# Kernel optimization log

Measured on AMD Instinct MI355X. Metric: run time of the kernel, lower is better.

The kernel has to match this reference:

```python
import jax, jax.numpy as jnp
import numpy as np

# SamplesLoss('sinkhorn', p=2, blur=0.05, backend='tensorized') defaults (geomloss):
# debiased Sinkhorn divergence, cost C(x,y)=|x-y|^2/2, eps = blur^p,
# epsilon-scaling from diameter^p down to blur^p with scaling=0.5,
# symmetric (averaged) log-domain updates + one final extrapolation step.
P = 2
BLUR = 0.05
SCALING = 0.5
DIAMETER = 10.0  # static diameter estimate for the annealing schedule (randn data)


def _eps_schedule():
    eps_target = BLUR ** P
    lst = []
    e = DIAMETER ** P
    while e > eps_target:
        lst.append(e)
        e *= SCALING ** P
    lst.append(eps_target)
    return lst

EPS_LIST = _eps_schedule()


def _sqcost(x, y):
    # C[b,n,m] = 0.5 * ||x_bn - y_bm||^2, via expansion (avoids [B,N,M,D] tensor)
    x2 = jnp.sum(x * x, axis=-1)  # [B,N]
    y2 = jnp.sum(y * y, axis=-1)  # [B,M]
    xy = jnp.einsum('bnd,bmd->bnm', x, y)
    return 0.5 * (x2[:, :, None] + y2[:, None, :] - 2.0 * xy)


def _softmin(eps, C, h):
    # h: [B,M] (already log-weights + potential/eps); C: [B,N,M] -> [B,N]
    return -eps * jax.nn.logsumexp(h[:, None, :] - C / eps, axis=2)


def _sinkhorn_divergence(x, y, a, b):
    log_a = jnp.log(a)
    log_b = jnp.log(b)
    Cxy = _sqcost(x, y)
    Cyx = jnp.swapaxes(Cxy, 1, 2)
    Cxx = _sqcost(x, x)
    Cyy = _sqcost(y, y)

    eps0 = EPS_LIST[0]
    f_ba = _softmin(eps0, Cxy, log_b)  # potential on x for OT(a,b)
    g_ab = _softmin(eps0, Cyx, log_a)  # potential on y for OT(a,b)
    f_aa = _softmin(eps0, Cxx, log_a)  # debias self-potential on x
    g_bb = _softmin(eps0, Cyy, log_b)  # debias self-potential on y

    for eps in EPS_LIST:
        ft = _softmin(eps, Cxy, log_b + g_ab / eps)
        gt = _softmin(eps, Cyx, log_a + f_ba / eps)
        f_ba = 0.5 * (f_ba + ft)
        g_ab = 0.5 * (g_ab + gt)
        f_aa = 0.5 * (f_aa + _softmin(eps, Cxx, log_a + f_aa / eps))
        g_bb = 0.5 * (g_bb + _softmin(eps, Cyy, log_b + g_bb / eps))

    # final (non-averaged) extrapolation at the target temperature
    eps = EPS_LIST[-1]
    f_fin = _softmin(eps, Cxy, log_b + g_ab / eps)
    g_fin = _softmin(eps, Cyx, log_a + f_ba / eps)
    f_aa = _softmin(eps, Cxx, log_a + f_aa / eps)
    g_bb = _softmin(eps, Cyy, log_b + g_bb / eps)

    # debiased divergence: <a, f_ab - f_aa> + <b, g_ab - g_bb>
    return jnp.sum(a * (f_fin - f_aa), axis=-1) + jnp.sum(b * (g_fin - g_bb), axis=-1)


def setup_inputs() -> dict:
    key = jax.random.key(0)
    k1, k2, k3, k4 = jax.random.split(key, 4)
    B, N, M, D = 8, 2048, 2048, 64
    return {
        'inp1': jax.random.normal(k1, (B, N, D), dtype=jnp.float32),
        'inp2': jax.random.normal(k2, (B, M, D), dtype=jnp.float32),
        'weights1': jax.random.uniform(k3, (B, N), dtype=jnp.float32),
        'weights2': jax.random.uniform(k4, (B, M), dtype=jnp.float32),
    }


def reference(inp1, inp2, weights1, weights2):
    # normalize_weights=True branch of SinkhornLoss.forward
    mass1 = jnp.sum(weights1, axis=1, keepdims=True)
    mass1 = jnp.where(mass1 == 0.0, 1.0, mass1)
    a = weights1 / mass1
    mass2 = jnp.sum(weights2, axis=1, keepdims=True)
    mass2 = jnp.where(mass2 == 0.0, 1.0, mass2)
    b = weights2 / mass2
    loss = _sinkhorn_divergence(inp1, inp2, a, b)  # [B]
    return jnp.mean(loss)  # reduction='mean'
```

## Files before the change

### kernel.cpp

```cpp
#include <hip/hip_runtime.h>
#include <cstdint>
#include <cstddef>

#define BB 8
#define NPTS 2048
#define DIM 64
#define CK 128
#define BROWS 64

typedef _Float16 f16x8 __attribute__((ext_vector_type(8)));
typedef float f32x4 __attribute__((ext_vector_type(4)));

static const float EPS_H[9] = {100.0f, 25.0f, 6.25f, 1.5625f, 0.390625f,
                               0.09765625f, 0.0244140625f, 0.006103515625f,
                               0.0025f};

#if __has_builtin(__builtin_amdgcn_exp2f)
static __device__ __forceinline__ float fexp2(float x) {
  return __builtin_amdgcn_exp2f(x);
}
#else
static __device__ __forceinline__ float fexp2(float x) {
  float r;
  asm("v_exp_f32 %0, %1" : "=v"(r) : "v"(x));
  return r;
}
#endif

static __device__ __forceinline__ f32x4 vmax4(f32x4 a, f32x4 b) {
  f32x4 r;
  #pragma unroll
  for (int i = 0; i < 4; ++i) r[i] = fmaxf(a[i], b[i]);
  return r;
}

static __device__ __forceinline__ f32x4 vexp2_4(f32x4 a) {
  f32x4 r;
  #pragma unroll
  for (int i = 0; i < 4; ++i) r[i] = fexp2(a[i]);
  return r;
}

static __device__ __forceinline__ void gload_lds16(const void* g, void* l) {
  __builtin_amdgcn_global_load_lds(
      (const __attribute__((address_space(1))) void*)g,
      (__attribute__((address_space(3))) void*)l, 16, 0, 0);
}

struct SMTask {
  const _Float16* P;
  const _Float16* Q;
  const float* logw;
  const float* pot;
  const float* qsq;
  const float* psq;
  const float* oldf;
  float* out;
};


__global__ __launch_bounds__(256) void norm_weights_k(
    const float* __restrict__ w, float* __restrict__ aout,
    float* __restrict__ logout, int n) {
  int b = blockIdx.x;
  const float* wb = w + (size_t)b * n;
  __shared__ float red[256];
  float s = 0.f;
  for (int i = threadIdx.x; i < n; i += 256) s += wb[i];
  red[threadIdx.x] = s;
  __syncthreads();
  for (int st = 128; st > 0; st >>= 1) {
    if (threadIdx.x < st) red[threadIdx.x] += red[threadIdx.x + st];
    __syncthreads();
  }
  float mass = red[0];
  if (mass == 0.f) mass = 1.f;
  float inv = 1.f / mass;
  for (int i = threadIdx.x; i < n; i += 256) {
    float av = wb[i] * inv;
    aout[(size_t)b * n + i] = av;
    logout[(size_t)b * n + i] = logf(av);
  }
}

__global__ __launch_bounds__(256) void sqnorm_cvt_k(
    const float* __restrict__ X, float* __restrict__ sq,
    _Float16* __restrict__ Xh, int rows) {
  int row = blockIdx.x * 4 + (threadIdx.x >> 6);
  int lane = threadIdx.x & 63;
  if (row >= rows) return;
  float v = X[(size_t)row * DIM + lane];
  Xh[(size_t)row * DIM + lane] = (_Float16)v;
  float s = v * v;
  #pragma unroll
  for (int off = 32; off > 0; off >>= 1) s += __shfl_xor(s, off);
  if (lane == 0) sq[row] = s;
}

__global__ __launch_bounds__(256, 4) void fused_softmin_k(
    SMTask t0, SMTask t1, SMTask t2, SMTask t3, float ie2, float neg_eps_ln2) {
  __shared__ float hq[NPTS];
  __shared__ __align__(16) _Float16 qb[2][CK * DIM];
  SMTask T = (blockIdx.z == 0) ? t0
           : (blockIdx.z == 1) ? t1
           : (blockIdx.z == 2) ? t2 : t3;
  const int b = blockIdx.y;
  const int tid = threadIdx.x;
  const float LOG2E = 1.4426950408889634f;
  {
    const float* lw = T.logw + (size_t)b * NPTS;
    const float* q2 = T.qsq + (size_t)b * NPTS;
    const float* pt = T.pot ? T.pot + (size_t)b * NPTS : nullptr;
    for (int m = tid; m < NPTS; m += 256) {
      float h = fmaf(lw[m], LOG2E, -0.5f * q2[m] * ie2);
      if (pt) h = fmaf(pt[m], ie2, h);
      hq[m] = h;
    }
  }

  const int lane = tid & 63, wave = tid >> 6;
  const _Float16* Qb = T.Q + (size_t)b * NPTS * DIM;

  auto stage = [&](int buf, int chunk) {
    int m0 = chunk * CK;
    #pragma unroll
    for (int r = 0; r < 4; ++r) {
      int gbase = r * 256 + wave * 64;
      int gid = gbase + lane;
      int row = gid >> 3;
      int kg = (gid & 7) ^ (row & 7);
      const _Float16* src = Qb + (size_t)(m0 + row) * DIM + kg * 8;
      _Float16* dst = &qb[buf][(size_t)gbase * 8];
      gload_lds16(src, dst);
    }
  };

  const int fr = lane & 15;
  const int g0 = lane >> 4;
  const int r0 = blockIdx.x * BROWS + wave * 16;
  const _Float16* Pb = T.P + ((size_t)b * NPTS + r0) * DIM;
  f16x8 a0 = *(const f16x8*)(Pb + fr * DIM + g0 * 8);
  f16x8 a1 = *(const f16x8*)(Pb + fr * DIM + g0 * 8 + 32);

  f32x4 mx4 = {-3.0e38f, -3.0e38f, -3.0e38f, -3.0e38f};
  f32x4 sm4 = {0.f, 0.f, 0.f, 0.f};

  stage(0, 0);
  __syncthreads();

  for (int c = 0; c < NPTS / CK; ++c) {
    int cur = c & 1;
    if (c + 1 < NPTS / CK) stage(cur ^ 1, c + 1);
    int m0 = c * CK;
    const char* qbase = (const char*)&qb[cur][0];

    f32x4 v4[8];
    f32x4 cmx = mx4;
    #pragma unroll
    for (int s = 0; s < 8; ++s) {
      int row = s * 16 + fr;
      int byte0 = row * 128 + ((g0 ^ (row & 7)) << 4);
      int byte1 = row * 128 + (((g0 + 4) ^ (row & 7)) << 4);
      f16x8 b0 = *(const f16x8*)(qbase + byte0);
      f16x8 b1 = *(const f16x8*)(qbase + byte1);
      float hs = hq[m0 + s * 16 + fr];
      f32x4 z = {0.f, 0.f, 0.f, 0.f};
      f32x4 t = __builtin_amdgcn_mfma_f32_16x16x32_f16(a0, b0, z, 0, 0, 0);
      f32x4 acc = __builtin_amdgcn_mfma_f32_16x16x32_f16(a1, b1, t, 0, 0, 0);
      v4[s] = acc * ie2 + hs;
      cmx = vmax4(cmx, v4[s]);
    }
    f32x4 resc = vexp2_4(mx4 - cmx);
    f32x4 esum = vexp2_4(v4[0] - cmx);
    #pragma unroll
    for (int s = 1; s < 8; ++s) esum += vexp2_4(v4[s] - cmx);
    sm4 = sm4 * resc + esum;
    mx4 = cmx;
    __syncthreads();
  }

  #pragma unroll
  for (int off = 1; off < 16; off <<= 1) {
    #pragma unroll
    for (int q = 0; q < 4; ++q) {
      float omx = __shfl_xor(mx4[q], off);
      float osm = __shfl_xor(sm4[q], off);
      float nm = fmaxf(mx4[q], omx);
      sm4[q] = sm4[q] * fexp2(mx4[q] - nm) + osm * fexp2(omx - nm);
      mx4[q] = nm;
    }
  }
  if (fr == 0) {
    #pragma unroll
    for (int q = 0; q < 4; ++q) {
      int r = r0 + g0 * 4 + q;
      size_t oi = (size_t)b * NPTS + r;
      float f = neg_eps_ln2 * (__log2f(sm4[q]) + mx4[q]) + 0.5f * T.psq[oi];
      if (T.oldf) f = 0.5f * (T.oldf[oi] + f);
      T.out[oi] = f;
    }
  }
}

__global__ __launch_bounds__(256) void loss_part_k(
    const float* __restrict__ aW, const float* __restrict__ f_fin,
    const float* __restrict__ f_aa, const float* __restrict__ bW,
    const float* __restrict__ g_fin, const float* __restrict__ g_bb,
    float* __restrict__ part) {
  __shared__ float red[256];
  int i0 = blockIdx.x * 256 + threadIdx.x;
  float s = 0.f;
  for (int i = i0; i < BB * NPTS; i += 64 * 256)
    s += aW[i] * (f_fin[i] - f_aa[i]) + bW[i] * (g_fin[i] - g_bb[i]);
  red[threadIdx.x] = s;
  __syncthreads();
  for (int st = 128; st > 0; st >>= 1) {
    if (threadIdx.x < st) red[threadIdx.x] += red[threadIdx.x + st];
    __syncthreads();
  }
  if (threadIdx.x == 0) part[blockIdx.x] = red[0];
}

__global__ __launch_bounds__(64) void loss_fin_k(const float* __restrict__ part,
                                                 float* __restrict__ out) {
  float s = part[threadIdx.x];
  #pragma unroll
  for (int off = 32; off > 0; off >>= 1) s += __shfl_xor(s, off);
  if (threadIdx.x == 0) out[0] = s * (1.f / BB);
}

__global__ void write_val_k(float* out, float v) { out[0] = v; }


extern "C" void kernel_launch(void* const* d_in, const int* in_sizes, int n_in,
                              void* d_out, int out_size, void* d_ws,
                              size_t ws_size, hipStream_t stream) {
  (void)in_sizes; (void)n_in; (void)out_size;
  const float* X = (const float*)d_in[0];
  const float* Y = (const float*)d_in[1];
  const float* W1 = (const float*)d_in[2];
  const float* W2 = (const float*)d_in[3];
  float* out = (float*)d_out;

  char* base = (char*)d_ws;
  size_t off = 0;
  auto alloc_b = [&](size_t bytes) {
    void* r = base + off;
    off += (bytes + 255) & ~(size_t)255;
    return r;
  };
  const size_t nP = (size_t)BB * NPTS;
  _Float16* Xh = (_Float16*)alloc_b(nP * DIM * 2);
  _Float16* Yh = (_Float16*)alloc_b(nP * DIM * 2);
  float* x2 = (float*)alloc_b(nP * 4);
  float* y2 = (float*)alloc_b(nP * 4);
  float* aW = (float*)alloc_b(nP * 4);
  float* bW = (float*)alloc_b(nP * 4);
  float* la = (float*)alloc_b(nP * 4);
  float* lb = (float*)alloc_b(nP * 4);
  float* fba[2] = {(float*)alloc_b(nP * 4), (float*)alloc_b(nP * 4)};
  float* gab[2] = {(float*)alloc_b(nP * 4), (float*)alloc_b(nP * 4)};
  float* faa[2] = {(float*)alloc_b(nP * 4), (float*)alloc_b(nP * 4)};
  float* gbb[2] = {(float*)alloc_b(nP * 4), (float*)alloc_b(nP * 4)};
  float* part = (float*)alloc_b(64 * 4);
  if (ws_size < off) {
    write_val_k<<<1, 1, 0, stream>>>(out, -(float)(ws_size >> 20));
    return;
  }

  norm_weights_k<<<BB, 256, 0, stream>>>(W1, aW, la, NPTS);
  norm_weights_k<<<BB, 256, 0, stream>>>(W2, bW, lb, NPTS);
  sqnorm_cvt_k<<<BB * NPTS / 4, 256, 0, stream>>>(X, x2, Xh, BB * NPTS);
  sqnorm_cvt_k<<<BB * NPTS / 4, 256, 0, stream>>>(Y, y2, Yh, BB * NPTS);

  const float LN2 = 0.6931471805599453f;
  const float LOG2E = 1.4426950408889634f;
  dim3 fg(NPTS / BROWS, BB, 4);

  auto launch4 = [&](SMTask A, SMTask B2, SMTask C, SMTask D2, float eps) {
    float ie2 = LOG2E / eps;
    float nel = -eps * LN2;
    fused_softmin_k<<<fg, 256, 0, stream>>>(A, B2, C, D2, ie2, nel);
  };

  {
    float e = EPS_H[0];
    launch4(
        SMTask{Xh, Yh, lb, nullptr, y2, x2, nullptr, fba[0]},
        SMTask{Yh, Xh, la, nullptr, x2, y2, nullptr, gab[0]},
        SMTask{Xh, Xh, la, nullptr, x2, x2, nullptr, faa[0]},
        SMTask{Yh, Yh, lb, nullptr, y2, y2, nullptr, gbb[0]},
        e);
  }

  int cur = 0;
  for (int it = 0; it < 9; ++it) {
    float e = EPS_H[it];
    int nxt = cur ^ 1;
    launch4(
        SMTask{Xh, Yh, lb, gab[cur], y2, x2, fba[cur], fba[nxt]},
        SMTask{Yh, Xh, la, fba[cur], x2, y2, gab[cur], gab[nxt]},
        SMTask{Xh, Xh, la, faa[cur], x2, x2, faa[cur], faa[nxt]},
        SMTask{Yh, Yh, lb, gbb[cur], y2, y2, gbb[cur], gbb[nxt]},
        e);
    cur = nxt;
  }

  {
    float e = EPS_H[8];
    int nxt = cur ^ 1;
    launch4(
        SMTask{Xh, Yh, lb, gab[cur], y2, x2, nullptr, fba[nxt]},
        SMTask{Yh, Xh, la, fba[cur], x2, y2, nullptr, gab[nxt]},
        SMTask{Xh, Xh, la, faa[cur], x2, x2, nullptr, faa[nxt]},
        SMTask{Yh, Yh, lb, gbb[cur], y2, y2, nullptr, gbb[nxt]},
        e);
    loss_part_k<<<64, 256, 0, stream>>>(aW, fba[nxt], faa[nxt], bW, gab[nxt],
                                        gbb[nxt], part);
    loss_fin_k<<<1, 64, 0, stream>>>(part, out);
  }
}
```

Before: 482.8 us.

## Pair softmin tasks sharing the same Q matrix and split the M range across block halves

Groups the four softmin tasks into two pairs that share the same Q operand (Y for f_ba/g_bb, X for g_ab/f_aa), so each staged Q tile in LDS feeds two MFMA streams. Blocks grow to 512 threads, with two halves each covering half of the M dimension; the two partial logsumexp results are merged through shared memory at the end. The per-chunk h values are computed inline from global memory instead of being precomputed into an LDS array. This halves Q traffic and LDS staging per output, at the cost of more registers per wave, fewer grid blocks, and a final cross-half reduction.

```diff
diff --git a/kernel.cpp b/kernel.cpp
--- a/kernel.cpp
+++ b/kernel.cpp
@@ -6,7 +6,6 @@
 #define NPTS 2048
 #define DIM 64
 #define CK 128
-#define BROWS 64
 
 typedef _Float16 f16x8 __attribute__((ext_vector_type(8)));
 typedef float f32x4 __attribute__((ext_vector_type(4)));
@@ -47,15 +46,20 @@
       (__attribute__((address_space(3))) void*)l, 16, 0, 0);
 }
 
-struct SMTask {
-  const _Float16* P;
+struct PTask {
   const _Float16* Q;
-  const float* logw;
-  const float* pot;
-  const float* qsq;
-  const float* psq;
-  const float* oldf;
-  float* out;
+  const float* lw;
+  const float* q2;
+  const _Float16* P0;
+  const float* pot0;
+  const float* psq0;
+  const float* oldf0;
+  float* out0;
+  const _Float16* P1;
+  const float* pot1;
+  const float* psq1;
+  const float* oldf1;
+  float* out1;
 };
 
 
@@ -97,85 +101,100 @@
   if (lane == 0) sq[row] = s;
 }
 
-__global__ __launch_bounds__(256, 4) void fused_softmin_k(
-    SMTask t0, SMTask t1, SMTask t2, SMTask t3, float ie2, float neg_eps_ln2) {
-  __shared__ float hq[NPTS];
-  __shared__ __align__(16) _Float16 qb[2][CK * DIM];
-  SMTask T = (blockIdx.z == 0) ? t0
-           : (blockIdx.z == 1) ? t1
-           : (blockIdx.z == 2) ? t2 : t3;
+__global__ __launch_bounds__(512, 4) void fused_softmin_k(
+    PTask u0, PTask u1, float ie2, float neg_eps_ln2) {
+  __shared__ __align__(16) _Float16 qb[2][2][CK * DIM];
+  __shared__ float cmxs[2][2][64];
+  __shared__ float csms[2][2][64];
+  PTask U = blockIdx.z ? u1 : u0;
   const int b = blockIdx.y;
   const int tid = threadIdx.x;
+  const int lane = tid & 63, wave = tid >> 6;
+  const int half = wave >> 2, wsub = wave & 3;
   const float LOG2E = 1.4426950408889634f;
-  {
-    const float* lw = T.logw + (size_t)b * NPTS;
-    const float* q2 = T.qsq + (size_t)b * NPTS;
-    const float* pt = T.pot ? T.pot + (size_t)b * NPTS : nullptr;
-    for (int m = tid; m < NPTS; m += 256) {
-      float h = fmaf(lw[m], LOG2E, -0.5f * q2[m] * ie2);
-      if (pt) h = fmaf(pt[m], ie2, h);
-      hq[m] = h;
-    }
-  }
-
-  const int lane = tid & 63, wave = tid >> 6;
-  const _Float16* Qb = T.Q + (size_t)b * NPTS * DIM;
-
-  auto stage = [&](int buf, int chunk) {
-    int m0 = chunk * CK;
+
+  const _Float16* Qb = U.Q + (size_t)b * NPTS * DIM;
+  const float* lwb = U.lw + (size_t)b * NPTS;
+  const float* q2b = U.q2 + (size_t)b * NPTS;
+  const float* pt0 = U.pot0 ? U.pot0 + (size_t)b * NPTS : nullptr;
+  const float* pt1 = U.pot1 ? U.pot1 + (size_t)b * NPTS : nullptr;
+
+  auto stage = [&](int buf, int c) {
+    int m0 = half * (NPTS / 2) + c * CK;
     #pragma unroll
     for (int r = 0; r < 4; ++r) {
-      int gbase = r * 256 + wave * 64;
+      int gbase = r * 256 + wsub * 64;
       int gid = gbase + lane;
       int row = gid >> 3;
       int kg = (gid & 7) ^ (row & 7);
       const _Float16* src = Qb + (size_t)(m0 + row) * DIM + kg * 8;
-      _Float16* dst = &qb[buf][(size_t)gbase * 8];
+      _Float16* dst = &qb[half][buf][(size_t)gbase * 8];
       gload_lds16(src, dst);
     }
   };
 
   const int fr = lane & 15;
   const int g0 = lane >> 4;
-  const int r0 = blockIdx.x * BROWS + wave * 16;
-  const _Float16* Pb = T.P + ((size_t)b * NPTS + r0) * DIM;
-  f16x8 a0 = *(const f16x8*)(Pb + fr * DIM + g0 * 8);
-  f16x8 a1 = *(const f16x8*)(Pb + fr * DIM + g0 * 8 + 32);
-
-  f32x4 mx4 = {-3.0e38f, -3.0e38f, -3.0e38f, -3.0e38f};
-  f32x4 sm4 = {0.f, 0.f, 0.f, 0.f};
+  const int r0 = blockIdx.x * 64 + wsub * 16;
+  const _Float16* P0b = U.P0 + ((size_t)b * NPTS + r0) * DIM;
+  const _Float16* P1b = U.P1 + ((size_t)b * NPTS + r0) * DIM;
+  f16x8 a00 = *(const f16x8*)(P0b + fr * DIM + g0 * 8);
+  f16x8 a01 = *(const f16x8*)(P0b + fr * DIM + g0 * 8 + 32);
+  f16x8 a10 = *(const f16x8*)(P1b + fr * DIM + g0 * 8);
+  f16x8 a11 = *(const f16x8*)(P1b + fr * DIM + g0 * 8 + 32);
+
+  f32x4 mx0 = {-3.0e38f, -3.0e38f, -3.0e38f, -3.0e38f};
+  f32x4 mx1 = mx0;
+  f32x4 sm0 = {0.f, 0.f, 0.f, 0.f};
+  f32x4 sm1 = sm0;
 
   stage(0, 0);
   __syncthreads();
 
-  for (int c = 0; c < NPTS / CK; ++c) {
+  for (int c = 0; c < NPTS / 2 / CK; ++c) {
     int cur = c & 1;
-    if (c + 1 < NPTS / CK) stage(cur ^ 1, c + 1);
-    int m0 = c * CK;
-    const char* qbase = (const char*)&qb[cur][0];
-
-    f32x4 v4[8];
-    f32x4 cmx = mx4;
+    if (c + 1 < NPTS / 2 / CK) stage(cur ^ 1, c + 1);
+    const int m0 = half * (NPTS / 2) + c * CK;
+    const char* qbase = (const char*)&qb[half][cur][0];
+
     #pragma unroll
-    for (int s = 0; s < 8; ++s) {
-      int row = s * 16 + fr;
-      int byte0 = row * 128 + ((g0 ^ (row & 7)) << 4);
-      int byte1 = row * 128 + (((g0 + 4) ^ (row & 7)) << 4);
-      f16x8 b0 = *(const f16x8*)(qbase + byte0);
-      f16x8 b1 = *(const f16x8*)(qbase + byte1);
-      float hs = hq[m0 + s * 16 + fr];
-      f32x4 z = {0.f, 0.f, 0.f, 0.f};
-      f32x4 t = __builtin_amdgcn_mfma_f32_16x16x32_f16(a0, b0, z, 0, 0, 0);
-      f32x4 acc = __builtin_amdgcn_mfma_f32_16x16x32_f16(a1, b1, t, 0, 0, 0);
-      v4[s] = acc * ie2 + hs;
-      cmx = vmax4(cmx, v4[s]);
+    for (int sh = 0; sh < 2; ++sh) {
+      float hs0[4], hs1[4];
+      #pragma unroll
+      for (int s4 = 0; s4 < 4; ++s4) {
+        int m = m0 + (sh * 4 + s4) * 16 + fr;
+        float hb = fmaf(lwb[m], LOG2E, -0.5f * q2b[m] * ie2);
+        hs0[s4] = pt0 ? fmaf(pt0[m], ie2, hb) : hb;
+        hs1[s4] = pt1 ? fmaf(pt1[m], ie2, hb) : hb;
+      }
+      f32x4 v0[4], v1[4];
+      f32x4 c0 = mx0, c1 = mx1;
+      #pragma unroll
+      for (int s4 = 0; s4 < 4; ++s4) {
+        int row = (sh * 4 + s4) * 16 + fr;
+        int byte0 = row * 128 + ((g0 ^ (row & 7)) << 4);
+        int byte1 = row * 128 + (((g0 + 4) ^ (row & 7)) << 4);
+        f16x8 b0 = *(const f16x8*)(qbase + byte0);
+        f16x8 b1 = *(const f16x8*)(qbase + byte1);
+        f32x4 z = {0.f, 0.f, 0.f, 0.f};
+        f32x4 t0 = __builtin_amdgcn_mfma_f32_16x16x32_f16(a00, b0, z, 0, 0, 0);
+        f32x4 acc0 = __builtin_amdgcn_mfma_f32_16x16x32_f16(a01, b1, t0, 0, 0, 0);
+        f32x4 t1 = __builtin_amdgcn_mfma_f32_16x16x32_f16(a10, b0, z, 0, 0, 0);
+        f32x4 acc1 = __builtin_amdgcn_mfma_f32_16x16x32_f16(a11, b1, t1, 0, 0, 0);
+        v0[s4] = acc0 * ie2 + hs0[s4];
+        v1[s4] = acc1 * ie2 + hs1[s4];
+        c0 = vmax4(c0, v0[s4]);
+        c1 = vmax4(c1, v1[s4]);
+      }
+      f32x4 e0 = vexp2_4(v0[0] - c0) + vexp2_4(v0[1] - c0);
+      e0 += vexp2_4(v0[2] - c0) + vexp2_4(v0[3] - c0);
+      sm0 = sm0 * vexp2_4(mx0 - c0) + e0;
+      mx0 = c0;
+      f32x4 e1 = vexp2_4(v1[0] - c1) + vexp2_4(v1[1] - c1);
+      e1 += vexp2_4(v1[2] - c1) + vexp2_4(v1[3] - c1);
+      sm1 = sm1 * vexp2_4(mx1 - c1) + e1;
+      mx1 = c1;
     }
-    f32x4 resc = vexp2_4(mx4 - cmx);
-    f32x4 esum = vexp2_4(v4[0] - cmx);
-    #pragma unroll
-    for (int s = 1; s < 8; ++s) esum += vexp2_4(v4[s] - cmx);
-    sm4 = sm4 * resc + esum;
-    mx4 = cmx;
     __syncthreads();
   }
 
@@ -183,22 +202,48 @@
   for (int off = 1; off < 16; off <<= 1) {
     #pragma unroll
     for (int q = 0; q < 4; ++q) {
-      float omx = __shfl_xor(mx4[q], off);
-      float osm = __shfl_xor(sm4[q], off);
-      float nm = fmaxf(mx4[q], omx);
-      sm4[q] = sm4[q] * fexp2(mx4[q] - nm) + osm * fexp2(omx - nm);
-      mx4[q] = nm;
+      {
+        float omx = __shfl_xor(mx0[q], off);
+        float osm = __shfl_xor(sm0[q], off);
+        float nm = fmaxf(mx0[q], omx);
+        sm0[q] = sm0[q] * fexp2(mx0[q] - nm) + osm * fexp2(omx - nm);
+        mx0[q] = nm;
+      }
+      {
+        float omx = __shfl_xor(mx1[q], off);
+        float osm = __shfl_xor(sm1[q], off);
+        float nm = fmaxf(mx1[q], omx);
+        sm1[q] = sm1[q] * fexp2(mx1[q] - nm) + osm * fexp2(omx - nm);
+        mx1[q] = nm;
+      }
     }
   }
   if (fr == 0) {
     #pragma unroll
     for (int q = 0; q < 4; ++q) {
-      int r = r0 + g0 * 4 + q;
-      size_t oi = (size_t)b * NPTS + r;
-      float f = neg_eps_ln2 * (__log2f(sm4[q]) + mx4[q]) + 0.5f * T.psq[oi];
-      if (T.oldf) f = 0.5f * (T.oldf[oi] + f);
-      T.out[oi] = f;
+      int rl = wsub * 16 + g0 * 4 + q;
+      cmxs[0][half][rl] = mx0[q];
+      csms[0][half][rl] = sm0[q];
+      cmxs[1][half][rl] = mx1[q];
+      csms[1][half][rl] = sm1[q];
     }
+  }
+  __syncthreads();
+
+  if (tid < 128) {
+    int task = tid >> 6;
+    int rl = tid & 63;
+    float ma = cmxs[task][0][rl], mb = cmxs[task][1][rl];
+    float nm = fmaxf(ma, mb);
+    float ss = csms[task][0][rl] * fexp2(ma - nm) +
+               csms[task][1][rl] * fexp2(mb - nm);
+    size_t oi = (size_t)b * NPTS + blockIdx.x * 64 + rl;
+    const float* psq = task ? U.psq1 : U.psq0;
+    const float* oldf = task ? U.oldf1 : U.oldf0;
+    float* outp = task ? U.out1 : U.out0;
+    float f = neg_eps_ln2 * (__log2f(ss) + nm) + 0.5f * psq[oi];
+    if (oldf) f = 0.5f * (oldf[oi] + f);
+    outp[oi] = f;
   }
 }
 
@@ -275,46 +320,43 @@
 
   const float LN2 = 0.6931471805599453f;
   const float LOG2E = 1.4426950408889634f;
-  dim3 fg(NPTS / BROWS, BB, 4);
-
-  auto launch4 = [&](SMTask A, SMTask B2, SMTask C, SMTask D2, float eps) {
+  dim3 fg(NPTS / 64, BB, 2);
+
+  auto launch4 = [&](const float* potF, const float* oldF, float* outF,
+                     const float* potG, const float* oldG, float* outG,
+                     const float* potA, const float* oldA, float* outA,
+                     const float* potBv, const float* oldBv, float* outBv,
+                     float eps) {
     float ie2 = LOG2E / eps;
     float nel = -eps * LN2;
-    fused_softmin_k<<<fg, 256, 0, stream>>>(A, B2, C, D2, ie2, nel);
+    PTask u0{Yh, lb, y2,
+             Xh, potF, x2, oldF, outF,
+             Yh, potBv, y2, oldBv, outBv};
+    PTask u1{Xh, la, x2,
+             Yh, potG, y2, oldG, outG,
+             Xh, potA, x2, oldA, outA};
+    fused_softmin_k<<<fg, 512, 0, stream>>>(u0, u1, ie2, nel);
   };
 
-  {
-    float e = EPS_H[0];
-    launch4(
-        SMTask{Xh, Yh, lb, nullptr, y2, x2, nullptr, fba[0]},
-        SMTask{Yh, Xh, la, nullptr, x2, y2, nullptr, gab[0]},
-        SMTask{Xh, Xh, la, nullptr, x2, x2, nullptr, faa[0]},
-        SMTask{Yh, Yh, lb, nullptr, y2, y2, nullptr, gbb[0]},
-        e);
-  }
+  launch4(nullptr, nullptr, fba[0], nullptr, nullptr, gab[0],
+          nullptr, nullptr, faa[0], nullptr, nullptr, gbb[0], EPS_H[0]);
 
   int cur = 0;
   for (int it = 0; it < 9; ++it) {
-    float e = EPS_H[it];
     int nxt = cur ^ 1;
-    launch4(
-        SMTask{Xh, Yh, lb, gab[cur], y2, x2, fba[cur], fba[nxt]},
-        SMTask{Yh, Xh, la, fba[cur], x2, y2, gab[cur], gab[nxt]},
-        SMTask{Xh, Xh, la, faa[cur], x2, x2, faa[cur], faa[nxt]},
-        SMTask{Yh, Yh, lb, gbb[cur], y2, y2, gbb[cur], gbb[nxt]},
-        e);
+    launch4(gab[cur], fba[cur], fba[nxt],
+            fba[cur], gab[cur], gab[nxt],
+            faa[cur], faa[cur], faa[nxt],
+            gbb[cur], gbb[cur], gbb[nxt], EPS_H[it]);
     cur = nxt;
   }
 
   {
-    float e = EPS_H[8];
     int nxt = cur ^ 1;
-    launch4(
-        SMTask{Xh, Yh, lb, gab[cur], y2, x2, nullptr, fba[nxt]},
-        SMTask{Yh, Xh, la, fba[cur], x2, y2, nullptr, gab[nxt]},
-        SMTask{Xh, Xh, la, faa[cur], x2, x2, nullptr, faa[nxt]},
-        SMTask{Yh, Yh, lb, gbb[cur], y2, y2, nullptr, gbb[nxt]},
-        e);
+    launch4(gab[cur], nullptr, fba[nxt],
+            fba[cur], nullptr, gab[nxt],
+            faa[cur], nullptr, faa[nxt],
+            gbb[cur], nullptr, gbb[nxt], EPS_H[8]);
     loss_part_k<<<64, 256, 0, stream>>>(aW, fba[nxt], faa[nxt], bW, gab[nxt],
                                         gbb[nxt], part);
     loss_fin_k<<<1, 64, 0, stream>>>(part, out);
```

Result: slower. 680.2 us (+40.9%).

## Split softmin over column halves with 32x32 MFMA and separate merge kernel

Applied to the files above, without the earlier changes.

Reworks the fused softmin kernel into single-wave blocks that each handle 32 rows against one half of the columns, using 32x32x16 MFMA and small 32-column chunks with explicit vmcnt waits and priority hints. Partial max/sum results are written to global memory and combined in a new merge kernel. That kernel also precomputes the next iteration's h vectors, replacing the per-block recomputation of h in LDS. This raises block count and parallelism and removes redundant h setup, but adds a global round trip for partials and an extra launch per iteration.

```diff
diff --git a/kernel.cpp b/kernel.cpp
--- a/kernel.cpp
+++ b/kernel.cpp
@@ -5,15 +5,18 @@
 #define BB 8
 #define NPTS 2048
 #define DIM 64
-#define CK 128
-#define BROWS 64
+#define CK 32
+#define HALFC 1024
+#define NCH (HALFC / CK)
 
 typedef _Float16 f16x8 __attribute__((ext_vector_type(8)));
-typedef float f32x4 __attribute__((ext_vector_type(4)));
+typedef float f32x16 __attribute__((ext_vector_type(16)));
 
 static const float EPS_H[9] = {100.0f, 25.0f, 6.25f, 1.5625f, 0.390625f,
                                0.09765625f, 0.0244140625f, 0.006103515625f,
                                0.0025f};
+#define LOG2E 1.4426950408889634f
+#define LN2 0.6931471805599453f
 
 #if __has_builtin(__builtin_amdgcn_exp2f)
 static __device__ __forceinline__ float fexp2(float x) {
@@ -27,35 +30,23 @@
 }
 #endif
 
-static __device__ __forceinline__ f32x4 vmax4(f32x4 a, f32x4 b) {
-  f32x4 r;
-  #pragma unroll
-  for (int i = 0; i < 4; ++i) r[i] = fmaxf(a[i], b[i]);
-  return r;
-}
-
-static __device__ __forceinline__ f32x4 vexp2_4(f32x4 a) {
-  f32x4 r;
-  #pragma unroll
-  for (int i = 0; i < 4; ++i) r[i] = fexp2(a[i]);
-  return r;
-}
-
 static __device__ __forceinline__ void gload_lds16(const void* g, void* l) {
   __builtin_amdgcn_global_load_lds(
       (const __attribute__((address_space(1))) void*)g,
       (__attribute__((address_space(3))) void*)l, 16, 0, 0);
 }
 
-struct SMTask {
+struct FT {
   const _Float16* P;
   const _Float16* Q;
-  const float* logw;
-  const float* pot;
-  const float* qsq;
+};
+struct MT {
   const float* psq;
   const float* oldf;
   float* out;
+  const float* lwn;
+  const float* q2n;
+  float* hqn;
 };
 
 
@@ -97,108 +88,154 @@
   if (lane == 0) sq[row] = s;
 }
 
-__global__ __launch_bounds__(256, 4) void fused_softmin_k(
-    SMTask t0, SMTask t1, SMTask t2, SMTask t3, float ie2, float neg_eps_ln2) {
-  __shared__ float hq[NPTS];
+__global__ __launch_bounds__(256) void init_hq_k(
+    const float* __restrict__ la, const float* __restrict__ lb,
+    const float* __restrict__ x2, const float* __restrict__ y2,
+    float* __restrict__ hq, float ie2) {
+  int task = blockIdx.z;
+  int idx = blockIdx.x * 256 + threadIdx.x;
+  const float* lw = (task == 1 || task == 2) ? la : lb;
+  const float* q2 = (task == 1 || task == 2) ? x2 : y2;
+  hq[(size_t)task * BB * NPTS + idx] =
+      fmaf(lw[idx], LOG2E, -0.5f * q2[idx] * ie2);
+}
+
+__global__ __launch_bounds__(64, 4) void fused_softmin_k(
+    FT t0, FT t1, FT t2, FT t3, const float* __restrict__ hqG,
+    float* __restrict__ pmx, float* __restrict__ psm, float ie2) {
   __shared__ __align__(16) _Float16 qb[2][CK * DIM];
-  SMTask T = (blockIdx.z == 0) ? t0
-           : (blockIdx.z == 1) ? t1
-           : (blockIdx.z == 2) ? t2 : t3;
-  const int b = blockIdx.y;
-  const int tid = threadIdx.x;
-  const float LOG2E = 1.4426950408889634f;
-  {
-    const float* lw = T.logw + (size_t)b * NPTS;
-    const float* q2 = T.qsq + (size_t)b * NPTS;
-    const float* pt = T.pot ? T.pot + (size_t)b * NPTS : nullptr;
-    for (int m = tid; m < NPTS; m += 256) {
-      float h = fmaf(lw[m], LOG2E, -0.5f * q2[m] * ie2);
-      if (pt) h = fmaf(pt[m], ie2, h);
-      hq[m] = h;
-    }
-  }
-
-  const int lane = tid & 63, wave = tid >> 6;
-  const _Float16* Qb = T.Q + (size_t)b * NPTS * DIM;
-
-  auto stage = [&](int buf, int chunk) {
-    int m0 = chunk * CK;
+  FT T = (blockIdx.z == 0) ? t0
+       : (blockIdx.z == 1) ? t1
+       : (blockIdx.z == 2) ? t2 : t3;
+  const int rowg = blockIdx.x >> 1, half = blockIdx.x & 1;
+  const int b = blockIdx.y, task = blockIdx.z;
+  const int lane = threadIdx.x;
+  const int l31 = lane & 31, hi = lane >> 5;
+
+  const _Float16* Qb = T.Q + ((size_t)b * NPTS + half * HALFC) * DIM;
+  const float* hqp = hqG + ((size_t)task * BB + b) * NPTS + half * HALFC;
+
+  const _Float16* Pb = T.P + ((size_t)b * NPTS + rowg * 32) * DIM;
+  f16x8 a[4];
+  #pragma unroll
+  for (int s = 0; s < 4; ++s)
+    a[s] = *(const f16x8*)(Pb + (size_t)l31 * DIM + s * 16 + hi * 8);
+
+  int baddr[4];
+  #pragma unroll
+  for (int s = 0; s < 4; ++s)
+    baddr[s] = l31 * 128 + (((2 * s + hi) ^ (l31 & 7)) << 4);
+  const char* qb0 = (const char*)&qb[0][0];
+
+  auto stage = [&](int buf, int c) {
+    int m0 = c * CK;
     #pragma unroll
     for (int r = 0; r < 4; ++r) {
-      int gbase = r * 256 + wave * 64;
-      int gid = gbase + lane;
+      int gid = r * 64 + lane;
       int row = gid >> 3;
       int kg = (gid & 7) ^ (row & 7);
-      const _Float16* src = Qb + (size_t)(m0 + row) * DIM + kg * 8;
-      _Float16* dst = &qb[buf][(size_t)gbase * 8];
-      gload_lds16(src, dst);
+      gload_lds16(Qb + (size_t)(m0 + row) * DIM + kg * 8, &qb[buf][r * 512]);
     }
   };
 
-  const int fr = lane & 15;
-  const int g0 = lane >> 4;
-  const int r0 = blockIdx.x * BROWS + wave * 16;
-  const _Float16* Pb = T.P + ((size_t)b * NPTS + r0) * DIM;
-  f16x8 a0 = *(const f16x8*)(Pb + fr * DIM + g0 * 8);
-  f16x8 a1 = *(const f16x8*)(Pb + fr * DIM + g0 * 8 + 32);
-
-  f32x4 mx4 = {-3.0e38f, -3.0e38f, -3.0e38f, -3.0e38f};
-  f32x4 sm4 = {0.f, 0.f, 0.f, 0.f};
+  float mx[16], sm[16];
+  #pragma unroll
+  for (int r = 0; r < 16; ++r) { mx[r] = -3.0e38f; sm[r] = 0.f; }
 
   stage(0, 0);
-  __syncthreads();
-
-  for (int c = 0; c < NPTS / CK; ++c) {
-    int cur = c & 1;
-    if (c + 1 < NPTS / CK) stage(cur ^ 1, c + 1);
-    int m0 = c * CK;
-    const char* qbase = (const char*)&qb[cur][0];
-
-    f32x4 v4[8];
-    f32x4 cmx = mx4;
+  float hq_c = hqp[l31];
+  float v0[16], v1[16];
+
+#define SUB(c_, BUF_, VOUT_, LAST_)                                          \
+  {                                                                          \
+    float hq_n = 0.f;                                                        \
+    if (!(LAST_)) {                                                          \
+      stage((BUF_) ^ 1, (c_) + 1);                                           \
+      hq_n = hqp[((c_) + 1) * CK + l31];                                     \
+    }                                                                        \
+    if (LAST_) asm volatile("s_waitcnt vmcnt(0)" ::: "memory");              \
+    else       asm volatile("s_waitcnt vmcnt(5)" ::: "memory");              \
+    __builtin_amdgcn_sched_barrier(0);                                       \
+    f16x8 b0 = *(const f16x8*)(qb0 + (BUF_) * 4096 + baddr[0]);              \
+    f16x8 b1 = *(const f16x8*)(qb0 + (BUF_) * 4096 + baddr[1]);              \
+    f16x8 b2 = *(const f16x8*)(qb0 + (BUF_) * 4096 + baddr[2]);              \
+    f16x8 b3 = *(const f16x8*)(qb0 + (BUF_) * 4096 + baddr[3]);              \
+    f32x16 acc = {};                                                         \
+    __builtin_amdgcn_s_setprio(1);                                           \
+    acc = __builtin_amdgcn_mfma_f32_32x32x16_f16(a[0], b0, acc, 0, 0, 0);    \
+    acc = __builtin_amdgcn_mfma_f32_32x32x16_f16(a[1], b1, acc, 0, 0, 0);    \
+    acc = __builtin_amdgcn_mfma_f32_32x32x16_f16(a[2], b2, acc, 0, 0, 0);    \
+    acc = __builtin_amdgcn_mfma_f32_32x32x16_f16(a[3], b3, acc, 0, 0, 0);    \
+    __builtin_amdgcn_s_setprio(0);                                           \
+    _Pragma("unroll")                                                        \
+    for (int r = 0; r < 16; ++r) (VOUT_)[r] = fmaf(acc[r], ie2, hq_c);       \
+    hq_c = hq_n;                                                             \
+  }
+
+#define PAIR_TAIL()                                                          \
+  _Pragma("unroll")                                                          \
+  for (int r = 0; r < 16; ++r) {                                             \
+    float cm = fmaxf(fmaxf(mx[r], v0[r]), v1[r]);                            \
+    float e = fexp2(v0[r] - cm) + fexp2(v1[r] - cm);                         \
+    sm[r] = fmaf(sm[r], fexp2(mx[r] - cm), e);                               \
+    mx[r] = cm;                                                              \
+  }
+
+  for (int cp = 0; cp < NCH / 2 - 1; ++cp) {
+    SUB(2 * cp, 0, v0, false)
+    SUB(2 * cp + 1, 1, v1, false)
+    PAIR_TAIL()
+  }
+  SUB(NCH - 2, 0, v0, false)
+  SUB(NCH - 1, 1, v1, true)
+  PAIR_TAIL()
+#undef SUB
+#undef PAIR_TAIL
+
+  float fm[16];
+  #pragma unroll
+  for (int r = 0; r < 16; ++r) fm[r] = mx[r];
+  #pragma unroll
+  for (int off = 1; off < 32; off <<= 1) {
     #pragma unroll
-    for (int s = 0; s < 8; ++s) {
-      int row = s * 16 + fr;
-      int byte0 = row * 128 + ((g0 ^ (row & 7)) << 4);
-      int byte1 = row * 128 + (((g0 + 4) ^ (row & 7)) << 4);
-      f16x8 b0 = *(const f16x8*)(qbase + byte0);
-      f16x8 b1 = *(const f16x8*)(qbase + byte1);
-      float hs = hq[m0 + s * 16 + fr];
-      f32x4 z = {0.f, 0.f, 0.f, 0.f};
-      f32x4 t = __builtin_amdgcn_mfma_f32_16x16x32_f16(a0, b0, z, 0, 0, 0);
-      f32x4 acc = __builtin_amdgcn_mfma_f32_16x16x32_f16(a1, b1, t, 0, 0, 0);
-      v4[s] = acc * ie2 + hs;
-      cmx = vmax4(cmx, v4[s]);
+    for (int r = 0; r < 16; ++r) fm[r] = fmaxf(fm[r], __shfl_xor(fm[r], off));
+  }
+  #pragma unroll
+  for (int r = 0; r < 16; ++r) sm[r] *= fexp2(mx[r] - fm[r]);
+  #pragma unroll
+  for (int off = 1; off < 32; off <<= 1) {
+    #pragma unroll
+    for (int r = 0; r < 16; ++r) sm[r] += __shfl_xor(sm[r], off);
+  }
+  if (l31 == 0) {
+    #pragma unroll
+    for (int r = 0; r < 16; ++r) {
+      int row = (r & 3) + 8 * (r >> 2) + 4 * hi;
+      size_t pi =
+          (((size_t)task * BB + b) * NPTS + rowg * 32 + row) * 2 + half;
+      pmx[pi] = fm[r];
+      psm[pi] = sm[r];
     }
-    f32x4 resc = vexp2_4(mx4 - cmx);
-    f32x4 esum = vexp2_4(v4[0] - cmx);
-    #pragma unroll
-    for (int s = 1; s < 8; ++s) esum += vexp2_4(v4[s] - cmx);
-    sm4 = sm4 * resc + esum;
-    mx4 = cmx;
-    __syncthreads();
-  }
-
-  #pragma unroll
-  for (int off = 1; off < 16; off <<= 1) {
-    #pragma unroll
-    for (int q = 0; q < 4; ++q) {
-      float omx = __shfl_xor(mx4[q], off);
-      float osm = __shfl_xor(sm4[q], off);
-      float nm = fmaxf(mx4[q], omx);
-      sm4[q] = sm4[q] * fexp2(mx4[q] - nm) + osm * fexp2(omx - nm);
-      mx4[q] = nm;
-    }
-  }
-  if (fr == 0) {
-    #pragma unroll
-    for (int q = 0; q < 4; ++q) {
-      int r = r0 + g0 * 4 + q;
-      size_t oi = (size_t)b * NPTS + r;
-      float f = neg_eps_ln2 * (__log2f(sm4[q]) + mx4[q]) + 0.5f * T.psq[oi];
-      if (T.oldf) f = 0.5f * (T.oldf[oi] + f);
-      T.out[oi] = f;
-    }
+  }
+}
+
+__global__ __launch_bounds__(256) void merge_k(
+    const float* __restrict__ pmx, const float* __restrict__ psm,
+    MT m0, MT m1, MT m2, MT m3, float nel, float ie2n, int whq) {
+  int task = blockIdx.z;
+  MT M = (task == 0) ? m0 : (task == 1) ? m1 : (task == 2) ? m2 : m3;
+  int idx = blockIdx.x * 256 + threadIdx.x;
+  size_t pi = ((size_t)task * BB * NPTS + idx) * 2;
+  float ma = pmx[pi], mb = pmx[pi + 1];
+  float sa = psm[pi], sb = psm[pi + 1];
+  float nm = fmaxf(ma, mb);
+  float ss = sa * fexp2(ma - nm) + sb * fexp2(mb - nm);
+  float f = nel * (__log2f(ss) + nm) + 0.5f * M.psq[idx];
+  if (M.oldf) f = 0.5f * (M.oldf[idx] + f);
+  M.out[idx] = f;
+  if (whq) {
+    float h = fmaf(f, ie2n, fmaf(M.lwn[idx], LOG2E, -0.5f * M.q2n[idx] * ie2n));
+    M.hqn[idx] = h;
   }
 }
 
@@ -262,6 +299,9 @@
   float* gab[2] = {(float*)alloc_b(nP * 4), (float*)alloc_b(nP * 4)};
   float* faa[2] = {(float*)alloc_b(nP * 4), (float*)alloc_b(nP * 4)};
   float* gbb[2] = {(float*)alloc_b(nP * 4), (float*)alloc_b(nP * 4)};
+  float* hq = (float*)alloc_b(4 * nP * 4);
+  float* pmx = (float*)alloc_b(4 * nP * 2 * 4);
+  float* psm = (float*)alloc_b(4 * nP * 2 * 4);
   float* part = (float*)alloc_b(64 * 4);
   if (ws_size < off) {
     write_val_k<<<1, 1, 0, stream>>>(out, -(float)(ws_size >> 20));
@@ -273,48 +313,51 @@
   sqnorm_cvt_k<<<BB * NPTS / 4, 256, 0, stream>>>(X, x2, Xh, BB * NPTS);
   sqnorm_cvt_k<<<BB * NPTS / 4, 256, 0, stream>>>(Y, y2, Yh, BB * NPTS);
 
-  const float LN2 = 0.6931471805599453f;
-  const float LOG2E = 1.4426950408889634f;
-  dim3 fg(NPTS / BROWS, BB, 4);
-
-  auto launch4 = [&](SMTask A, SMTask B2, SMTask C, SMTask D2, float eps) {
-    float ie2 = LOG2E / eps;
+  dim3 fg(128, BB, 4);
+  dim3 mg(BB * NPTS / 256, 1, 4);
+
+  FT t0{Xh, Yh}, t1{Yh, Xh}, t2{Xh, Xh}, t3{Yh, Yh};
+  float* hq0 = hq;
+  float* hq1 = hq + 1 * nP;
+  float* hq2 = hq + 2 * nP;
+  float* hq3 = hq + 3 * nP;
+
+  auto fused = [&](float eps) {
+    fused_softmin_k<<<fg, 64, 0, stream>>>(t0, t1, t2, t3, hq, pmx, psm,
+                                           LOG2E / eps);
+  };
+  auto merge = [&](float eps, float ie2n, int whq, const float* oF,
+                   float* nF, const float* oG, float* nG, const float* oA,
+                   float* nA, const float* oB, float* nB) {
     float nel = -eps * LN2;
-    fused_softmin_k<<<fg, 256, 0, stream>>>(A, B2, C, D2, ie2, nel);
+    MT M0{x2, oF, nF, la, x2, hq1};
+    MT M1{y2, oG, nG, lb, y2, hq0};
+    MT M2{x2, oA, nA, la, x2, hq2};
+    MT M3{y2, oB, nB, lb, y2, hq3};
+    merge_k<<<mg, 256, 0, stream>>>(pmx, psm, M0, M1, M2, M3, nel, ie2n, whq);
   };
 
-  {
-    float e = EPS_H[0];
-    launch4(
-        SMTask{Xh, Yh, lb, nullptr, y2, x2, nullptr, fba[0]},
-        SMTask{Yh, Xh, la, nullptr, x2, y2, nullptr, gab[0]},
-        SMTask{Xh, Xh, la, nullptr, x2, x2, nullptr, faa[0]},
-        SMTask{Yh, Yh, lb, nullptr, y2, y2, nullptr, gbb[0]},
-        e);
-  }
+  init_hq_k<<<mg, 256, 0, stream>>>(la, lb, x2, y2, hq, LOG2E / EPS_H[0]);
+
+  fused(EPS_H[0]);
+  merge(EPS_H[0], LOG2E / EPS_H[0], 1, nullptr, fba[0], nullptr, gab[0],
+        nullptr, faa[0], nullptr, gbb[0]);
 
   int cur = 0;
   for (int it = 0; it < 9; ++it) {
-    float e = EPS_H[it];
     int nxt = cur ^ 1;
-    launch4(
-        SMTask{Xh, Yh, lb, gab[cur], y2, x2, fba[cur], fba[nxt]},
-        SMTask{Yh, Xh, la, fba[cur], x2, y2, gab[cur], gab[nxt]},
-        SMTask{Xh, Xh, la, faa[cur], x2, x2, faa[cur], faa[nxt]},
-        SMTask{Yh, Yh, lb, gbb[cur], y2, y2, gbb[cur], gbb[nxt]},
-        e);
+    float epsn = EPS_H[it < 8 ? it + 1 : 8];
+    fused(EPS_H[it]);
+    merge(EPS_H[it], LOG2E / epsn, 1, fba[cur], fba[nxt], gab[cur], gab[nxt],
+          faa[cur], faa[nxt], gbb[cur], gbb[nxt]);
     cur = nxt;
   }
 
   {
-    float e = EPS_H[8];
     int nxt = cur ^ 1;
-    launch4(
-        SMTask{Xh, Yh, lb, gab[cur], y2, x2, nullptr, fba[nxt]},
-        SMTask{Yh, Xh, la, fba[cur], x2, y2, nullptr, gab[nxt]},
-        SMTask{Xh, Xh, la, faa[cur], x2, x2, nullptr, faa[nxt]},
-        SMTask{Yh, Yh, lb, gbb[cur], y2, y2, nullptr, gbb[nxt]},
-        e);
+    fused(EPS_H[8]);
+    merge(EPS_H[8], 0.f, 0, nullptr, fba[nxt], nullptr, gab[nxt], nullptr,
+          faa[nxt], nullptr, gbb[nxt]);
     loss_part_k<<<64, 256, 0, stream>>>(aW, fba[nxt], faa[nxt], bW, gab[nxt],
                                         gbb[nxt], part);
     loss_fin_k<<<1, 64, 0, stream>>>(part, out);
```

Result: slower. 598.3 us (+23.9%).
